# Optimization experiments

Hardware: AMD Instinct MI355X
Metric: run time of the kernel (lower is better)

Reference implementation:

```python
import jax, jax.numpy as jnp
import numpy as np

N = 100000   # num nodes
E = 20000    # num hyperedges
D = 128      # feature dim
NNZ = 600000 # incidences
EPS = 1e-5


def setup_inputs() -> dict:
    key = jax.random.key(0)
    ks = jax.random.split(key, 16)
    src = jax.random.randint(ks[0], (NNZ,), 0, N)   # node indices
    edg = jax.random.randint(ks[1], (NNZ,), 0, E)   # hyperedge indices
    edge_index = jnp.stack([src, edg]).astype(jnp.int64)
    node_attr = jax.random.normal(ks[2], (N, D), jnp.float32)
    edge_attr = jax.random.normal(ks[3], (E, D), jnp.float32)  # unused by forward
    inp = {"edge_index": edge_index, "node_attr": node_attr, "edge_attr": edge_attr}
    for l in range(3):
        inp[f"W{l+1}"] = jax.random.normal(ks[4 + l], (D, D), jnp.float32) / np.float32(np.sqrt(D))
        inp[f"b{l+1}"] = jnp.zeros((D,), jnp.float32)
        inp[f"g{l+1}"] = jnp.ones((D,), jnp.float32)
        inp[f"beta{l+1}"] = jnp.zeros((D,), jnp.float32)
    return inp


def _hconv(x, W, b, src, edg):
    # PyG HypergraphConv (no attention): out = D^{-1} H W_e B^{-1} H^T (X Theta) + b, W_e = I
    x = x @ W
    ones = jnp.ones(src.shape, x.dtype)
    deg_n = jax.ops.segment_sum(ones, src, num_segments=N)  # node degree
    deg_e = jax.ops.segment_sum(ones, edg, num_segments=E)  # hyperedge size
    Dinv = jnp.where(deg_n > 0, 1.0 / deg_n, 0.0)
    Binv = jnp.where(deg_e > 0, 1.0 / deg_e, 0.0)
    # node -> hyperedge: m_e = B^{-1} sum_{i in e} x_i
    e_feat = Binv[:, None] * jax.ops.segment_sum(x[src], edg, num_segments=E)
    # hyperedge -> node: out_i = D^{-1} sum_{e ni i} m_e
    out = Dinv[:, None] * jax.ops.segment_sum(e_feat[edg], src, num_segments=N)
    return out + b


def _bn(x, g, beta):
    # BatchNorm1d, training mode (biased variance over nodes)
    mu = jnp.mean(x, axis=0)
    var = jnp.mean((x - mu) ** 2, axis=0)
    return g * (x - mu) / jnp.sqrt(var + EPS) + beta


def reference(edge_index, node_attr, edge_attr,
              W1, b1, g1, beta1, W2, b2, g2, beta2, W3, b3, g3, beta3):
    src, edg = edge_index[0], edge_index[1]
    x = _bn(jax.nn.relu(_hconv(node_attr, W1, b1, src, edg)), g1, beta1)
    x = _bn(jax.nn.relu(_hconv(x, W2, b2, src, edg)), g2, beta2)
    x = _bn(jax.nn.relu(_hconv(x, W3, b3, src, edg)), g3, beta3)
    return x
```

## Files before the change

kernel.cpp:

```cpp
#include <hip/hip_runtime.h>
#include <stdint.h>

#define DIM 128

static inline int cdiv(long a, long b) { return (int)((a + b - 1) / b); }

typedef float f32x4 __attribute__((ext_vector_type(4)));

__device__ __forceinline__ unsigned pk_bf16(float a, float b) {
  unsigned ua = __float_as_uint(a), ub = __float_as_uint(b);
  ua = (ua + 0x7FFFu + ((ua >> 16) & 1u)) >> 16;
  ub = (ub + 0x7FFFu + ((ub >> 16) & 1u)) >> 16;
  return ua | (ub << 16);
}
__device__ __forceinline__ float bf_lo(unsigned u) { return __uint_as_float(u << 16); }
__device__ __forceinline__ float bf_hi(unsigned u) { return __uint_as_float(u & 0xFFFF0000u); }

__device__ __forceinline__ void acc8(float4& a, const uint2* q) {
  a.x += ((bf_lo(q[0].x) + bf_lo(q[1].x)) + (bf_lo(q[2].x) + bf_lo(q[3].x))) +
         ((bf_lo(q[4].x) + bf_lo(q[5].x)) + (bf_lo(q[6].x) + bf_lo(q[7].x)));
  a.y += ((bf_hi(q[0].x) + bf_hi(q[1].x)) + (bf_hi(q[2].x) + bf_hi(q[3].x))) +
         ((bf_hi(q[4].x) + bf_hi(q[5].x)) + (bf_hi(q[6].x) + bf_hi(q[7].x)));
  a.z += ((bf_lo(q[0].y) + bf_lo(q[1].y)) + (bf_lo(q[2].y) + bf_lo(q[3].y))) +
         ((bf_lo(q[4].y) + bf_lo(q[5].y)) + (bf_lo(q[6].y) + bf_lo(q[7].y)));
  a.w += ((bf_hi(q[0].y) + bf_hi(q[1].y)) + (bf_hi(q[2].y) + bf_hi(q[3].y))) +
         ((bf_hi(q[4].y) + bf_hi(q[5].y)) + (bf_hi(q[6].y) + bf_hi(q[7].y)));
}

__global__ __launch_bounds__(256) void count_kernel(
    const int* __restrict__ raw, int* __restrict__ src, int* __restrict__ edg,
    int* __restrict__ cnt, int E, int nnz) {
  bool is64;
  {
    int l = threadIdx.x & 63;
    int v = raw[2 * l + 1];
    unsigned long long m = __ballot(v == 0);
    is64 = (m == ~0ull);
  }
  int g = blockIdx.x * 256 + threadIdx.x;
  if (g < nnz) {
    int s = is64 ? raw[2 * g] : raw[g];
    int e = is64 ? raw[2 * (nnz + g)] : raw[nnz + g];
    src[g] = s;
    edg[g] = e;
    atomicAdd(&cnt[e], 1);
    atomicAdd(&cnt[E + s], 1);
  }
}

__global__ __launch_bounds__(256) void scanA_kernel(
    const int* __restrict__ cnt, int* __restrict__ P, int* __restrict__ BS, int M) {
  __shared__ int lds[256];
  int t = threadIdx.x;
  long base = blockIdx.x * 1024L;
  int v[4], ts = 0;
#pragma unroll
  for (int j = 0; j < 4; ++j) {
    long i = base + t * 4 + j;
    v[j] = (i < M) ? cnt[i] : 0;
    ts += v[j];
  }
  lds[t] = ts;
  __syncthreads();
  for (int off = 1; off < 256; off <<= 1) {
    int x = (t >= off) ? lds[t - off] : 0;
    __syncthreads();
    lds[t] += x;
    __syncthreads();
  }
  int run = lds[t] - ts;
#pragma unroll
  for (int j = 0; j < 4; ++j) {
    long i = base + t * 4 + j;
    if (i < M) P[i] = run;
    run += v[j];
  }
  if (t == 255) BS[blockIdx.x] = lds[255];
}

__global__ void scanB_kernel(int* __restrict__ BS, int* __restrict__ P,
                             int nblocks, int M) {
  if (threadIdx.x == 0) {
    int run = 0;
    for (int i = 0; i < nblocks; ++i) { int x = BS[i]; BS[i] = run; run += x; }
    P[M] = run;
  }
}

__global__ __launch_bounds__(256) void scanC_kernel(
    int* __restrict__ P, const int* __restrict__ BS, int* __restrict__ cnt, int M) {
  long i = blockIdx.x * 256L + threadIdx.x;
  if (i < M) {
    P[i] += BS[i >> 10];
    cnt[i] = 0;
  }
}

__global__ __launch_bounds__(256) void fill_adj_kernel(
    const int* __restrict__ src, const int* __restrict__ edg,
    const int* __restrict__ P, int* __restrict__ cnt,
    int* __restrict__ adj_e, int* __restrict__ adj_n, int E, int N, int nnz) {
  int p = blockIdx.x & 7;
  int chunk = blockIdx.x >> 3;
  int e_lo = (int)(((long)E * p) >> 3), e_hi = (int)(((long)E * (p + 1)) >> 3);
  int s_lo = (int)(((long)N * p) >> 3), s_hi = (int)(((long)N * (p + 1)) >> 3);
  int base = chunk * 1024 + threadIdx.x;
#pragma unroll
  for (int it = 0; it < 4; ++it) {
    int g = base + it * 256;
    if (g < nnz) {
      int e = edg[g], s = src[g];
      if (e >= e_lo && e < e_hi) {
        int pe = P[e] + atomicAdd(&cnt[e], 1);
        adj_e[pe] = s;
      }
      if (s >= s_lo && s < s_hi) {
        int pn = P[E + s] - nnz + atomicAdd(&cnt[E + s], 1);
        adj_n[pn] = e;
      }
    }
  }
}

__global__ __launch_bounds__(1024) void prep_w_kernel(
    const float* __restrict__ W, float* __restrict__ sums,
    float* __restrict__ sumsq, const float* __restrict__ gprev,
    const float* __restrict__ betaprev, float* __restrict__ Wp,
    float* __restrict__ rvec, int has_aff, float inv_n) {
  __shared__ float sa[DIM], sd[DIM];
  __shared__ float red[1024];
  int t = threadIdx.x;
  if (t < DIM) {
    float a = 1.0f, d = 0.0f;
    if (has_aff) {
      float mu = sums[t] * inv_n;
      float var = fmaf(sumsq[t], inv_n, -mu * mu);
      a = gprev[t] * rsqrtf(var + 1e-5f);
      d = fmaf(-mu, a, betaprev[t]);
    }
    sa[t] = a; sd[t] = d;
  }
  __syncthreads();
  if (t < DIM) { sums[t] = 0.f; sumsq[t] = 0.f; }
  int j = t & 127, grp = t >> 7;
  float racc = 0.f;
  for (int c = grp; c < DIM; c += 8) {
    float w = W[c * DIM + j];
    Wp[c * DIM + j] = sa[c] * w;
    racc = fmaf(sd[c], w, racc);
  }
  red[t] = racc;
  __syncthreads();
  if (t < DIM) {
    float r = 0.f;
#pragma unroll
    for (int g2 = 0; g2 < 8; ++g2) r += red[j + g2 * 128];
    rvec[j] = r;
  }
}

__global__ __launch_bounds__(256) void edge_gather_f32_kernel(
    const float4* __restrict__ X4, const int* __restrict__ P,
    const int* __restrict__ adj_e, float* __restrict__ ag, int E) {
  int slot = threadIdx.x >> 5;
  int l = threadIdx.x & 31;
  int e = blockIdx.x * 8 + slot;
  if (e >= E) return;
  int p0 = P[e], p1 = P[e + 1];
  float4 a = {0.f, 0.f, 0.f, 0.f};
  int kl = p1 - 1;
  for (int k = p0; k < p1; k += 8) {
    int n0 = adj_e[min(k, kl)];
    int n1 = adj_e[min(k + 1, kl)];
    int n2 = adj_e[min(k + 2, kl)];
    int n3 = adj_e[min(k + 3, kl)];
    int n4 = adj_e[min(k + 4, kl)];
    int n5 = adj_e[min(k + 5, kl)];
    int n6 = adj_e[min(k + 6, kl)];
    int n7 = adj_e[min(k + 7, kl)];
    float4 q0 = X4[(size_t)n0 * 32 + l];
    float4 q1 = X4[(size_t)n1 * 32 + l];
    float4 q2 = X4[(size_t)n2 * 32 + l];
    float4 q3 = X4[(size_t)n3 * 32 + l];
    float4 q4 = X4[(size_t)n4 * 32 + l];
    float4 q5 = X4[(size_t)n5 * 32 + l];
    float4 q6 = X4[(size_t)n6 * 32 + l];
    float4 q7 = X4[(size_t)n7 * 32 + l];
    a.x += ((q0.x + q1.x) + (q2.x + q3.x)) + ((q4.x + q5.x) + (q6.x + q7.x));
    a.y += ((q0.y + q1.y) + (q2.y + q3.y)) + ((q4.y + q5.y) + (q6.y + q7.y));
    a.z += ((q0.z + q1.z) + (q2.z + q3.z)) + ((q4.z + q5.z) + (q6.z + q7.z));
    a.w += ((q0.w + q1.w) + (q2.w + q3.w)) + ((q4.w + q5.w) + (q6.w + q7.w));
  }
  int deg = p1 - p0;
  if (deg > 0) {
    int extra = ((deg + 7) & ~7) - deg;
    if (extra) {
      float4 ql = X4[(size_t)adj_e[kl] * 32 + l];
      float ex = (float)extra;
      a.x -= ex * ql.x; a.y -= ex * ql.y; a.z -= ex * ql.z; a.w -= ex * ql.w;
    }
  }
  float binv = (deg > 0) ? 1.0f / (float)deg : 0.0f;
  f32x4 o;
  o.x = a.x * binv; o.y = a.y * binv; o.z = a.z * binv; o.w = a.w * binv;
  __builtin_nontemporal_store(o, &((f32x4*)ag)[(size_t)e * 32 + l]);
}

__global__ __launch_bounds__(256) void edge_gather_bf16_kernel(
    const uint2* __restrict__ xh, const int* __restrict__ P,
    const int* __restrict__ adj_e, float* __restrict__ ag, int E, int SENT) {
  int slot = threadIdx.x >> 5;
  int l = threadIdx.x & 31;
  int e = blockIdx.x * 8 + slot;
  if (e >= E) return;
  int p0 = P[e], p1 = P[e + 1];
  float4 a = {0.f, 0.f, 0.f, 0.f};
  int kl = p1 - 1;
  for (int k = p0; k < p1; k += 16) {
    int n[16];
    n[0] = adj_e[k];
#pragma unroll
    for (int j = 1; j < 16; ++j) n[j] = (k + j <= kl) ? adj_e[k + j] : SENT;
    uint2 q[16];
#pragma unroll
    for (int j = 0; j < 16; ++j) q[j] = xh[(size_t)n[j] * 32 + l];
    acc8(a, q);
    acc8(a, q + 8);
  }
  int deg = p1 - p0;
  float binv = (deg > 0) ? 1.0f / (float)deg : 0.0f;
  f32x4 o;
  o.x = a.x * binv; o.y = a.y * binv; o.z = a.z * binv; o.w = a.w * binv;
  __builtin_nontemporal_store(o, &((f32x4*)ag)[(size_t)e * 32 + l]);
}

__global__ __launch_bounds__(256) void gemm128_kernel(
    const float* __restrict__ X, const float* __restrict__ Wp,
    const float* __restrict__ rvec, const int* __restrict__ Pdeg,
    unsigned* __restrict__ Yh, int nrows) {
  __shared__ float sW[32 * DIM];
  __shared__ float sX[DIM * 36];
  const int t = threadIdx.x;
  const int row0 = blockIdx.x * DIM;
  const int tx = t & 15, ty = t >> 4;
  const int col0 = tx * 8, lr0 = ty * 8;
  float acc[8][8];
#pragma unroll
  for (int i = 0; i < 8; ++i)
#pragma unroll
    for (int j = 0; j < 8; ++j) acc[i][j] = 0.0f;

  for (int kc = 0; kc < 4; ++kc) {
    __syncthreads();
    {
      const float4* W4 = (const float4*)(Wp + kc * 32 * DIM);
      float4* sW4 = (float4*)sW;
#pragma unroll
      for (int i = 0; i < 4; ++i) sW4[t + i * 256] = W4[t + i * 256];
    }
#pragma unroll
    for (int i = 0; i < 4; ++i) {
      int q = t + i * 256;
      int rr = q >> 3, kq = q & 7;
      int gr = row0 + rr; if (gr >= nrows) gr = nrows - 1;
      float4 v = *(const float4*)&X[(size_t)gr * DIM + kc * 32 + kq * 4];
      *(float4*)&sX[rr * 36 + kq * 4] = v;
    }
    __syncthreads();
    for (int kk = 0; kk < 32; ++kk) {
      float4 w0 = *(const float4*)&sW[kk * DIM + col0];
      float4 w1 = *(const float4*)&sW[kk * DIM + col0 + 4];
      float wv[8] = {w0.x, w0.y, w0.z, w0.w, w1.x, w1.y, w1.z, w1.w};
      float xv[8];
#pragma unroll
      for (int i = 0; i < 8; ++i) xv[i] = sX[(lr0 + i) * 36 + kk];
#pragma unroll
      for (int i = 0; i < 8; ++i)
#pragma unroll
        for (int j = 0; j < 8; ++j) acc[i][j] = fmaf(xv[i], wv[j], acc[i][j]);
    }
  }
  float4 r0 = *(const float4*)&rvec[col0];
  float4 r1 = *(const float4*)&rvec[col0 + 4];
#pragma unroll
  for (int i = 0; i < 8; ++i) {
    int gr = row0 + lr0 + i;
    if (gr < nrows) {
      float nz = (Pdeg[gr + 1] > Pdeg[gr]) ? 1.0f : 0.0f;
      float o0x = (acc[i][0] + r0.x) * nz, o0y = (acc[i][1] + r0.y) * nz;
      float o0z = (acc[i][2] + r0.z) * nz, o0w = (acc[i][3] + r0.w) * nz;
      float o1x = (acc[i][4] + r1.x) * nz, o1y = (acc[i][5] + r1.y) * nz;
      float o1z = (acc[i][6] + r1.z) * nz, o1w = (acc[i][7] + r1.w) * nz;
      uint4 st;
      st.x = pk_bf16(o0x, o0y);
      st.y = pk_bf16(o0z, o0w);
      st.z = pk_bf16(o1x, o1y);
      st.w = pk_bf16(o1z, o1w);
      *(uint4*)&Yh[(size_t)gr * 64 + (col0 >> 1)] = st;
    }
  }
}

__global__ __launch_bounds__(256) void node_gather_kernel(
    const uint2* __restrict__ ef, const int* __restrict__ P,
    const int* __restrict__ adj_n, const float* __restrict__ b,
    uint2* __restrict__ zh, float* __restrict__ sum,
    float* __restrict__ sumsq, int E, int N, int nnz, int SENT) {
  __shared__ float lsum[DIM], lsumsq[DIM];
  int t = threadIdx.x;
  if (t < DIM) { lsum[t] = 0.f; lsumsq[t] = 0.f; }
  __syncthreads();
  int slot = t >> 5;
  int l = t & 31;
  float4 bc = ((const float4*)b)[l];
  float4 s1 = {0.f, 0.f, 0.f, 0.f}, s2 = {0.f, 0.f, 0.f, 0.f};
  for (int i = blockIdx.x * 8 + slot; i < N; i += gridDim.x * 8) {
    int p0 = P[E + i] - nnz, p1 = P[E + i + 1] - nnz;
    float4 a = {0.f, 0.f, 0.f, 0.f};
    int kl = p1 - 1;
    for (int k = p0; k < p1; k += 8) {
      int e0 = adj_n[k];
      int e1 = (k + 1 <= kl) ? adj_n[k + 1] : SENT;
      int e2 = (k + 2 <= kl) ? adj_n[k + 2] : SENT;
      int e3 = (k + 3 <= kl) ? adj_n[k + 3] : SENT;
      int e4 = (k + 4 <= kl) ? adj_n[k + 4] : SENT;
      int e5 = (k + 5 <= kl) ? adj_n[k + 5] : SENT;
      int e6 = (k + 6 <= kl) ? adj_n[k + 6] : SENT;
      int e7 = (k + 7 <= kl) ? adj_n[k + 7] : SENT;
      uint2 q[8];
      q[0] = ef[(size_t)e0 * 32 + l];
      q[1] = ef[(size_t)e1 * 32 + l];
      q[2] = ef[(size_t)e2 * 32 + l];
      q[3] = ef[(size_t)e3 * 32 + l];
      q[4] = ef[(size_t)e4 * 32 + l];
      q[5] = ef[(size_t)e5 * 32 + l];
      q[6] = ef[(size_t)e6 * 32 + l];
      q[7] = ef[(size_t)e7 * 32 + l];
      acc8(a, q);
    }
    int deg = p1 - p0;
    float dinv = (deg > 0) ? 1.0f / (float)deg : 0.0f;
    float4 v;
    v.x = fmaxf(fmaf(dinv, a.x, bc.x), 0.f);
    v.y = fmaxf(fmaf(dinv, a.y, bc.y), 0.f);
    v.z = fmaxf(fmaf(dinv, a.z, bc.z), 0.f);
    v.w = fmaxf(fmaf(dinv, a.w, bc.w), 0.f);
    uint2 o;
    o.x = pk_bf16(v.x, v.y);
    o.y = pk_bf16(v.z, v.w);
    zh[(size_t)i * 32 + l] = o;
    s1.x += v.x; s1.y += v.y; s1.z += v.z; s1.w += v.w;
    s2.x = fmaf(v.x, v.x, s2.x); s2.y = fmaf(v.y, v.y, s2.y);
    s2.z = fmaf(v.z, v.z, s2.z); s2.w = fmaf(v.w, v.w, s2.w);
  }
  int c0 = l * 4;
  atomicAdd(&lsum[c0 + 0], s1.x); atomicAdd(&lsum[c0 + 1], s1.y);
  atomicAdd(&lsum[c0 + 2], s1.z); atomicAdd(&lsum[c0 + 3], s1.w);
  atomicAdd(&lsumsq[c0 + 0], s2.x); atomicAdd(&lsumsq[c0 + 1], s2.y);
  atomicAdd(&lsumsq[c0 + 2], s2.z); atomicAdd(&lsumsq[c0 + 3], s2.w);
  __syncthreads();
  if (t < DIM) {
    atomicAdd(&sum[t], lsum[t]);
    atomicAdd(&sumsq[t], lsumsq[t]);
  }
}

__global__ __launch_bounds__(256) void apply_affine_kernel(
    const uint2* __restrict__ zh, const float* __restrict__ sums,
    const float* __restrict__ sumsq, const float* __restrict__ g,
    const float* __restrict__ beta, float* __restrict__ out,
    long total4, float inv_n) {
  __shared__ float sa[DIM], sd[DIM];
  int t = threadIdx.x;
  if (t < DIM) {
    float mu = sums[t] * inv_n;
    float var = fmaf(sumsq[t], inv_n, -mu * mu);
    float a = g[t] * rsqrtf(var + 1e-5f);
    sa[t] = a;
    sd[t] = fmaf(-mu, a, beta[t]);
  }
  __syncthreads();
  long i = blockIdx.x * 256L + t;
  if (i >= total4) return;
  int c0 = (int)(i & 31) * 4;
  uint2 q = zh[i];
  f32x4 o;
  o.x = fmaf(sa[c0 + 0], bf_lo(q.x), sd[c0 + 0]);
  o.y = fmaf(sa[c0 + 1], bf_hi(q.x), sd[c0 + 1]);
  o.z = fmaf(sa[c0 + 2], bf_lo(q.y), sd[c0 + 2]);
  o.w = fmaf(sa[c0 + 3], bf_hi(q.y), sd[c0 + 3]);
  __builtin_nontemporal_store(o, &((f32x4*)out)[i]);
}

extern "C" void kernel_launch(void* const* d_in, const int* in_sizes, int n_in,
                              void* d_out, int out_size, void* d_ws, size_t ws_size,
                              hipStream_t stream) {
  const int NNZv = in_sizes[0] / 2;
  const int Nv   = in_sizes[1] / DIM;
  const int Ev   = in_sizes[2] / DIM;
  const int* eidx_raw = (const int*)d_in[0];
  const float* node_attr = (const float*)d_in[1];

  float* bufE  = (float*)d_ws;
  float* Wp    = bufE + (size_t)Ev * DIM;
  float* rvec  = Wp + DIM * DIM;
  float* sums  = rvec + 128;
  float* sumsq = sums + 128;
  float* aff_a = sumsq + 128;
  float* aff_d = aff_a + 128;
  int* src   = (int*)(aff_d + 128);
  int* edg   = src + NNZv;
  int* cnt   = edg + NNZv;
  int* P     = cnt + (((size_t)Ev + Nv + 3) & ~(size_t)3);
  int* BS    = P + (((size_t)Ev + Nv + 1 + 3) & ~(size_t)3);
  int* adj_e = BS + 256;
  int* adj_n = adj_e + NNZv;
  unsigned* efh = (unsigned*)src;
  uint2* xh = (uint2*)(adj_n + NNZv);

  const int M = Ev + Nv;
  const int nbA = cdiv(M, 1024);
  const float inv_n = 1.0f / (float)Nv;

  hipMemsetAsync(cnt, 0, (size_t)M * 4, stream);
  count_kernel<<<cdiv(NNZv, 256), 256, 0, stream>>>(eidx_raw, src, edg, cnt, Ev, NNZv);
  scanA_kernel<<<nbA, 256, 0, stream>>>(cnt, P, BS, M);
  scanB_kernel<<<1, 64, 0, stream>>>(BS, P, nbA, M);
  scanC_kernel<<<cdiv(M, 256), 256, 0, stream>>>(P, BS, cnt, M);
  fill_adj_kernel<<<cdiv(NNZv, 1024) * 8, 256, 0, stream>>>(
      src, edg, P, cnt, adj_e, adj_n, Ev, Nv, NNZv);
  hipMemsetAsync(efh + (size_t)Ev * 64, 0, 256, stream);
  hipMemsetAsync(xh + (size_t)Nv * 32, 0, 256, stream);

  for (int l = 0; l < 3; ++l) {
    const float* W     = (const float*)d_in[3 + l * 4];
    const float* b     = (const float*)d_in[4 + l * 4];
    const float* gprev    = (const float*)d_in[5 + (l > 0 ? l - 1 : 0) * 4];
    const float* betaprev = (const float*)d_in[6 + (l > 0 ? l - 1 : 0) * 4];

    prep_w_kernel<<<1, 1024, 0, stream>>>(W, sums, sumsq, gprev, betaprev,
                                          Wp, rvec, l > 0 ? 1 : 0, inv_n);
    if (l == 0)
      edge_gather_f32_kernel<<<cdiv(Ev, 8), 256, 0, stream>>>(
          (const float4*)node_attr, P, adj_e, bufE, Ev);
    else
      edge_gather_bf16_kernel<<<cdiv(Ev, 8), 256, 0, stream>>>(
          xh, P, adj_e, bufE, Ev, Nv);
    gemm128_kernel<<<cdiv(Ev, DIM), 256, 0, stream>>>(bufE, Wp, rvec, P, efh, Ev);
    node_gather_kernel<<<2048, 256, 0, stream>>>(
        (const uint2*)efh, P, adj_n, b, xh, sums, sumsq, Ev, Nv, NNZv, Ev);
  }
  {
    const float* g2    = (const float*)d_in[5 + 2 * 4];
    const float* beta2 = (const float*)d_in[6 + 2 * 4];
    apply_affine_kernel<<<cdiv((long)Nv * 32, 256), 256, 0, stream>>>(
        xh, sums, sumsq, g2, beta2, (float*)d_out, (long)Nv * 32, inv_n);
  }
}
```

Measured before the change: 673.4 us.

## Fuse hyperedge gather with 128x128 projection, dropping separate GEMM kernel

The hyperedge mean-aggregation kernels now stage each edge's aggregated row in shared memory and immediately multiply it by the prepared weight matrix, writing bf16 edge features directly. This removes the fp32 intermediate edge buffer write and read plus one kernel launch per layer. The trade-off is that each warp streams the full weight matrix from global/L2 with no register tiling, so the GEMM part does less data reuse than the tiled kernel it replaces.

```diff
diff --git a/kernel.cpp b/kernel.cpp
--- a/kernel.cpp
+++ b/kernel.cpp
@@ -159,146 +159,126 @@
   }
 }
 
-__global__ __launch_bounds__(256) void edge_gather_f32_kernel(
+
+__global__ __launch_bounds__(256) void edge_fused_f32_kernel(
     const float4* __restrict__ X4, const int* __restrict__ P,
-    const int* __restrict__ adj_e, float* __restrict__ ag, int E) {
+    const int* __restrict__ adj_e, const float* __restrict__ Wp,
+    const float* __restrict__ rvec, unsigned* __restrict__ Yh, int E) {
+  __shared__ float sag[8][132];
   int slot = threadIdx.x >> 5;
   int l = threadIdx.x & 31;
   int e = blockIdx.x * 8 + slot;
+  float4 a = {0.f, 0.f, 0.f, 0.f};
+  int deg = 0;
+  if (e < E) {
+    int p0 = P[e], p1 = P[e + 1];
+    deg = p1 - p0;
+    int kl = p1 - 1;
+    for (int k = p0; k < p1; k += 8) {
+      int n0 = adj_e[min(k, kl)];
+      int n1 = adj_e[min(k + 1, kl)];
+      int n2 = adj_e[min(k + 2, kl)];
+      int n3 = adj_e[min(k + 3, kl)];
+      int n4 = adj_e[min(k + 4, kl)];
+      int n5 = adj_e[min(k + 5, kl)];
+      int n6 = adj_e[min(k + 6, kl)];
+      int n7 = adj_e[min(k + 7, kl)];
+      float4 q0 = X4[(size_t)n0 * 32 + l];
+      float4 q1 = X4[(size_t)n1 * 32 + l];
+      float4 q2 = X4[(size_t)n2 * 32 + l];
+      float4 q3 = X4[(size_t)n3 * 32 + l];
+      float4 q4 = X4[(size_t)n4 * 32 + l];
+      float4 q5 = X4[(size_t)n5 * 32 + l];
+      float4 q6 = X4[(size_t)n6 * 32 + l];
+      float4 q7 = X4[(size_t)n7 * 32 + l];
+      a.x += ((q0.x + q1.x) + (q2.x + q3.x)) + ((q4.x + q5.x) + (q6.x + q7.x));
+      a.y += ((q0.y + q1.y) + (q2.y + q3.y)) + ((q4.y + q5.y) + (q6.y + q7.y));
+      a.z += ((q0.z + q1.z) + (q2.z + q3.z)) + ((q4.z + q5.z) + (q6.z + q7.z));
+      a.w += ((q0.w + q1.w) + (q2.w + q3.w)) + ((q4.w + q5.w) + (q6.w + q7.w));
+    }
+    if (deg > 0) {
+      int extra = ((deg + 7) & ~7) - deg;
+      if (extra) {
+        float4 ql = X4[(size_t)adj_e[kl] * 32 + l];
+        float ex = (float)extra;
+        a.x -= ex * ql.x; a.y -= ex * ql.y; a.z -= ex * ql.z; a.w -= ex * ql.w;
+      }
+      float binv = 1.0f / (float)deg;
+      a.x *= binv; a.y *= binv; a.z *= binv; a.w *= binv;
+    }
+  }
+  *(float4*)&sag[slot][l * 4] = a;
+  __syncthreads();
   if (e >= E) return;
-  int p0 = P[e], p1 = P[e + 1];
-  float4 a = {0.f, 0.f, 0.f, 0.f};
-  int kl = p1 - 1;
-  for (int k = p0; k < p1; k += 8) {
-    int n0 = adj_e[min(k, kl)];
-    int n1 = adj_e[min(k + 1, kl)];
-    int n2 = adj_e[min(k + 2, kl)];
-    int n3 = adj_e[min(k + 3, kl)];
-    int n4 = adj_e[min(k + 4, kl)];
-    int n5 = adj_e[min(k + 5, kl)];
-    int n6 = adj_e[min(k + 6, kl)];
-    int n7 = adj_e[min(k + 7, kl)];
-    float4 q0 = X4[(size_t)n0 * 32 + l];
-    float4 q1 = X4[(size_t)n1 * 32 + l];
-    float4 q2 = X4[(size_t)n2 * 32 + l];
-    float4 q3 = X4[(size_t)n3 * 32 + l];
-    float4 q4 = X4[(size_t)n4 * 32 + l];
-    float4 q5 = X4[(size_t)n5 * 32 + l];
-    float4 q6 = X4[(size_t)n6 * 32 + l];
-    float4 q7 = X4[(size_t)n7 * 32 + l];
-    a.x += ((q0.x + q1.x) + (q2.x + q3.x)) + ((q4.x + q5.x) + (q6.x + q7.x));
-    a.y += ((q0.y + q1.y) + (q2.y + q3.y)) + ((q4.y + q5.y) + (q6.y + q7.y));
-    a.z += ((q0.z + q1.z) + (q2.z + q3.z)) + ((q4.z + q5.z) + (q6.z + q7.z));
-    a.w += ((q0.w + q1.w) + (q2.w + q3.w)) + ((q4.w + q5.w) + (q6.w + q7.w));
-  }
-  int deg = p1 - p0;
-  if (deg > 0) {
-    int extra = ((deg + 7) & ~7) - deg;
-    if (extra) {
-      float4 ql = X4[(size_t)adj_e[kl] * 32 + l];
-      float ex = (float)extra;
-      a.x -= ex * ql.x; a.y -= ex * ql.y; a.z -= ex * ql.z; a.w -= ex * ql.w;
-    }
-  }
-  float binv = (deg > 0) ? 1.0f / (float)deg : 0.0f;
-  f32x4 o;
-  o.x = a.x * binv; o.y = a.y * binv; o.z = a.z * binv; o.w = a.w * binv;
-  __builtin_nontemporal_store(o, &((f32x4*)ag)[(size_t)e * 32 + l]);
-}
-
-__global__ __launch_bounds__(256) void edge_gather_bf16_kernel(
+  float4 r = ((const float4*)rvec)[l];
+  float4 acc = {0.f, 0.f, 0.f, 0.f};
+  const float4* W4 = (const float4*)Wp;
+#pragma unroll 8
+  for (int c = 0; c < DIM; ++c) {
+    float av = sag[slot][c];
+    float4 w = W4[c * 32 + l];
+    acc.x = fmaf(av, w.x, acc.x);
+    acc.y = fmaf(av, w.y, acc.y);
+    acc.z = fmaf(av, w.z, acc.z);
+    acc.w = fmaf(av, w.w, acc.w);
+  }
+  float nz = (deg > 0) ? 1.0f : 0.0f;
+  uint2 st;
+  st.x = pk_bf16((acc.x + r.x) * nz, (acc.y + r.y) * nz);
+  st.y = pk_bf16((acc.z + r.z) * nz, (acc.w + r.w) * nz);
+  ((uint2*)Yh)[(size_t)e * 32 + l] = st;
+}
+
+__global__ __launch_bounds__(256) void edge_fused_bf16_kernel(
     const uint2* __restrict__ xh, const int* __restrict__ P,
-    const int* __restrict__ adj_e, float* __restrict__ ag, int E, int SENT) {
+    const int* __restrict__ adj_e, const float* __restrict__ Wp,
+    const float* __restrict__ rvec, unsigned* __restrict__ Yh, int E, int SENT) {
+  __shared__ float sag[8][132];
   int slot = threadIdx.x >> 5;
   int l = threadIdx.x & 31;
   int e = blockIdx.x * 8 + slot;
+  float4 a = {0.f, 0.f, 0.f, 0.f};
+  int deg = 0;
+  if (e < E) {
+    int p0 = P[e], p1 = P[e + 1];
+    deg = p1 - p0;
+    int kl = p1 - 1;
+    for (int k = p0; k < p1; k += 16) {
+      int n[16];
+      n[0] = adj_e[k];
+#pragma unroll
+      for (int j = 1; j < 16; ++j) n[j] = (k + j <= kl) ? adj_e[k + j] : SENT;
+      uint2 q[16];
+#pragma unroll
+      for (int j = 0; j < 16; ++j) q[j] = xh[(size_t)n[j] * 32 + l];
+      acc8(a, q);
+      acc8(a, q + 8);
+    }
+    if (deg > 0) {
+      float binv = 1.0f / (float)deg;
+      a.x *= binv; a.y *= binv; a.z *= binv; a.w *= binv;
+    }
+  }
+  *(float4*)&sag[slot][l * 4] = a;
+  __syncthreads();
   if (e >= E) return;
-  int p0 = P[e], p1 = P[e + 1];
-  float4 a = {0.f, 0.f, 0.f, 0.f};
-  int kl = p1 - 1;
-  for (int k = p0; k < p1; k += 16) {
-    int n[16];
-    n[0] = adj_e[k];
-#pragma unroll
-    for (int j = 1; j < 16; ++j) n[j] = (k + j <= kl) ? adj_e[k + j] : SENT;
-    uint2 q[16];
-#pragma unroll
-    for (int j = 0; j < 16; ++j) q[j] = xh[(size_t)n[j] * 32 + l];
-    acc8(a, q);
-    acc8(a, q + 8);
-  }
-  int deg = p1 - p0;
-  float binv = (deg > 0) ? 1.0f / (float)deg : 0.0f;
-  f32x4 o;
-  o.x = a.x * binv; o.y = a.y * binv; o.z = a.z * binv; o.w = a.w * binv;
-  __builtin_nontemporal_store(o, &((f32x4*)ag)[(size_t)e * 32 + l]);
-}
-
-__global__ __launch_bounds__(256) void gemm128_kernel(
-    const float* __restrict__ X, const float* __restrict__ Wp,
-    const float* __restrict__ rvec, const int* __restrict__ Pdeg,
-    unsigned* __restrict__ Yh, int nrows) {
-  __shared__ float sW[32 * DIM];
-  __shared__ float sX[DIM * 36];
-  const int t = threadIdx.x;
-  const int row0 = blockIdx.x * DIM;
-  const int tx = t & 15, ty = t >> 4;
-  const int col0 = tx * 8, lr0 = ty * 8;
-  float acc[8][8];
-#pragma unroll
-  for (int i = 0; i < 8; ++i)
-#pragma unroll
-    for (int j = 0; j < 8; ++j) acc[i][j] = 0.0f;
-
-  for (int kc = 0; kc < 4; ++kc) {
-    __syncthreads();
-    {
-      const float4* W4 = (const float4*)(Wp + kc * 32 * DIM);
-      float4* sW4 = (float4*)sW;
-#pragma unroll
-      for (int i = 0; i < 4; ++i) sW4[t + i * 256] = W4[t + i * 256];
-    }
-#pragma unroll
-    for (int i = 0; i < 4; ++i) {
-      int q = t + i * 256;
-      int rr = q >> 3, kq = q & 7;
-      int gr = row0 + rr; if (gr >= nrows) gr = nrows - 1;
-      float4 v = *(const float4*)&X[(size_t)gr * DIM + kc * 32 + kq * 4];
-      *(float4*)&sX[rr * 36 + kq * 4] = v;
-    }
-    __syncthreads();
-    for (int kk = 0; kk < 32; ++kk) {
-      float4 w0 = *(const float4*)&sW[kk * DIM + col0];
-      float4 w1 = *(const float4*)&sW[kk * DIM + col0 + 4];
-      float wv[8] = {w0.x, w0.y, w0.z, w0.w, w1.x, w1.y, w1.z, w1.w};
-      float xv[8];
-#pragma unroll
-      for (int i = 0; i < 8; ++i) xv[i] = sX[(lr0 + i) * 36 + kk];
-#pragma unroll
-      for (int i = 0; i < 8; ++i)
-#pragma unroll
-        for (int j = 0; j < 8; ++j) acc[i][j] = fmaf(xv[i], wv[j], acc[i][j]);
-    }
-  }
-  float4 r0 = *(const float4*)&rvec[col0];
-  float4 r1 = *(const float4*)&rvec[col0 + 4];
-#pragma unroll
-  for (int i = 0; i < 8; ++i) {
-    int gr = row0 + lr0 + i;
-    if (gr < nrows) {
-      float nz = (Pdeg[gr + 1] > Pdeg[gr]) ? 1.0f : 0.0f;
-      float o0x = (acc[i][0] + r0.x) * nz, o0y = (acc[i][1] + r0.y) * nz;
-      float o0z = (acc[i][2] + r0.z) * nz, o0w = (acc[i][3] + r0.w) * nz;
-      float o1x = (acc[i][4] + r1.x) * nz, o1y = (acc[i][5] + r1.y) * nz;
-      float o1z = (acc[i][6] + r1.z) * nz, o1w = (acc[i][7] + r1.w) * nz;
-      uint4 st;
-      st.x = pk_bf16(o0x, o0y);
-      st.y = pk_bf16(o0z, o0w);
-      st.z = pk_bf16(o1x, o1y);
-      st.w = pk_bf16(o1z, o1w);
-      *(uint4*)&Yh[(size_t)gr * 64 + (col0 >> 1)] = st;
-    }
-  }
+  float4 r = ((const float4*)rvec)[l];
+  float4 acc = {0.f, 0.f, 0.f, 0.f};
+  const float4* W4 = (const float4*)Wp;
+#pragma unroll 8
+  for (int c = 0; c < DIM; ++c) {
+    float av = sag[slot][c];
+    float4 w = W4[c * 32 + l];
+    acc.x = fmaf(av, w.x, acc.x);
+    acc.y = fmaf(av, w.y, acc.y);
+    acc.z = fmaf(av, w.z, acc.z);
+    acc.w = fmaf(av, w.w, acc.w);
+  }
+  float nz = (deg > 0) ? 1.0f : 0.0f;
+  uint2 st;
+  st.x = pk_bf16((acc.x + r.x) * nz, (acc.y + r.y) * nz);
+  st.y = pk_bf16((acc.z + r.z) * nz, (acc.w + r.w) * nz);
+  ((uint2*)Yh)[(size_t)e * 32 + l] = st;
 }
 
 __global__ __launch_bounds__(256) void node_gather_kernel(
@@ -401,14 +381,12 @@
   const int* eidx_raw = (const int*)d_in[0];
   const float* node_attr = (const float*)d_in[1];
 
-  float* bufE  = (float*)d_ws;
-  float* Wp    = bufE + (size_t)Ev * DIM;
+  float* Wp    = (float*)d_ws;
   float* rvec  = Wp + DIM * DIM;
   float* sums  = rvec + 128;
   float* sumsq = sums + 128;
-  float* aff_a = sumsq + 128;
-  float* aff_d = aff_a + 128;
-  int* src   = (int*)(aff_d + 128);
+  float* pad0  = sumsq + 128;
+  int* src   = (int*)(pad0 + 256);
   int* edg   = src + NNZv;
   int* cnt   = edg + NNZv;
   int* P     = cnt + (((size_t)Ev + Nv + 3) & ~(size_t)3);
@@ -441,12 +419,11 @@
     prep_w_kernel<<<1, 1024, 0, stream>>>(W, sums, sumsq, gprev, betaprev,
                                           Wp, rvec, l > 0 ? 1 : 0, inv_n);
     if (l == 0)
-      edge_gather_f32_kernel<<<cdiv(Ev, 8), 256, 0, stream>>>(
-          (const float4*)node_attr, P, adj_e, bufE, Ev);
+      edge_fused_f32_kernel<<<cdiv(Ev, 8), 256, 0, stream>>>(
+          (const float4*)node_attr, P, adj_e, Wp, rvec, efh, Ev);
     else
-      edge_gather_bf16_kernel<<<cdiv(Ev, 8), 256, 0, stream>>>(
-          xh, P, adj_e, bufE, Ev, Nv);
-    gemm128_kernel<<<cdiv(Ev, DIM), 256, 0, stream>>>(bufE, Wp, rvec, P, efh, Ev);
+      edge_fused_bf16_kernel<<<cdiv(Ev, 8), 256, 0, stream>>>(
+          xh, P, adj_e, Wp, rvec, efh, Ev, Nv);
     node_gather_kernel<<<2048, 256, 0, stream>>>(
         (const uint2*)efh, P, adj_n, b, xh, sums, sumsq, Ev, Nv, NNZv, Ev);
   }
```

Measured after the change: 695.9 us. 3.3% more time.
